# Performance work log

Measured on AMD Instinct MI355X. Metric: run time of the kernel, lower is better.

## Reference

```python
import jax, jax.numpy as jnp
import numpy as np

B, S = 2, 2048
DIM_IN, DIM_OUT, NUM_HEADS, DIM_QK = 1024, 128, 16, 128


def setup_inputs() -> dict:
    key = jax.random.key(0)
    k0, k1, k2, k3 = jax.random.split(key, 4)
    x = jax.random.normal(k0, (B, S, DIM_IN), jnp.float32)
    mask = jax.random.bernoulli(k1, 0.1, (B, S))  # True = masked-out token
    # xavier-normal-ish scales (exact init values are irrelevant for correctness)
    std_in = float(np.sqrt(2.0 / (NUM_HEADS * DIM_QK + DIM_IN * DIM_QK)))
    proj_in = jax.random.normal(k2, (DIM_IN, NUM_HEADS, 2 * DIM_QK + DIM_OUT), jnp.float32) * std_in
    v_bias = jnp.zeros((NUM_HEADS, DIM_OUT), jnp.float32)
    std_out = float(np.sqrt(2.0 / (DIM_OUT * DIM_OUT + NUM_HEADS * DIM_OUT)))
    proj_out = jax.random.normal(k3, (NUM_HEADS, DIM_OUT, DIM_OUT), jnp.float32) * std_out
    proj_out_bias = jnp.zeros((DIM_OUT,), jnp.float32)
    return {"x": x, "mask": mask, "proj_in": proj_in, "v_bias": v_bias,
            "proj_out": proj_out, "proj_out_bias": proj_out_bias}


def _rotary(t):
    # t: [z, s, h, d]; GPT-NeoX style rotary as in the torch Rotary module
    d = t.shape[-1]
    half = -(-d // 2)  # ceil(d/2), matches torch.arange(0,-1,-2/d)
    freq_half = 10000.0 ** (jnp.arange(half, dtype=jnp.float32) * (-2.0 / d))
    freq = jnp.concatenate([freq_half, freq_half[: half - d % 2]])  # length d
    pos = jnp.arange(t.shape[1], dtype=jnp.float32)
    ang = pos[:, None] * freq[None, :]             # [s, d]
    cos = jnp.cos(ang)[None, :, None, :]
    sin = jnp.sin(ang)[None, :, None, :]
    x1, x2 = jnp.split(t, 2, axis=-1)
    rot = jnp.concatenate([-x2, x1], axis=-1)
    return t * cos + rot * sin


def _inf_cube(t):
    return t ** 3


def reference(x, mask, proj_in, v_bias, proj_out, proj_out_bias):
    qkv = jnp.einsum('zki,iho->zkho', x, proj_in)
    q, k, v = jnp.split(qkv, [DIM_QK, 2 * DIM_QK], axis=-1)
    q = _rotary(q)
    k = _rotary(k)
    scores = jnp.einsum('zqha,zkha->zqkh', q, k) / jnp.sqrt(jnp.float32(DIM_QK))
    # dual mask: row (query) OR column (key) masked -> -inf
    m = jnp.logical_or(mask[:, :, None, None], mask[:, None, :, None])  # [z,q,k,1]
    scores = jnp.where(m, -jnp.inf, scores)
    attn = jnp.nan_to_num(jax.nn.softmax(scores, axis=2))  # softmax over k; nan rows -> 0
    o = jnp.einsum('zqkh,zkhx->zqhx', attn, v + v_bias[None, None])
    out = jnp.einsum('zqhx,hxy->zqy', _inf_cube(o), proj_out) + proj_out_bias[None, None]
    return _inf_cube(out)
```

## Files before the change

### kernel.cpp

```cpp
#include <hip/hip_runtime.h>
#include <math.h>

#define BZ 2
#define SQ 2048
#define DIN 1024
#define HH 16
#define NT 6144
#define MROWS 4096
#define KOUT 2048
#define KSPLIT 16

typedef unsigned short u16t;
typedef unsigned int u32t;
typedef __attribute__((ext_vector_type(8))) short bf16x8;
typedef __attribute__((ext_vector_type(4))) float f32x4;

__device__ __forceinline__ float cubef(float x) { return x * x * x; }

__device__ __forceinline__ u16t f2bf(float f) {
    u32t b = __float_as_uint(f);
    b += 0x7FFFu + ((b >> 16) & 1u);
    return (u16t)(b >> 16);
}
__device__ __forceinline__ float bf2f(u16t u) { return __uint_as_float(((u32t)u) << 16); }
__device__ __forceinline__ u32t pk2(float a, float b) {
    return (u32t)f2bf(a) | ((u32t)f2bf(b) << 16);
}

#if __has_builtin(__builtin_amdgcn_exp2f)
#define EXP2(x) __builtin_amdgcn_exp2f(x)
#else
#define EXP2(x) exp2f(x)
#endif

__device__ __forceinline__ void load_lds16(const void* g, void* l) {
    __builtin_amdgcn_global_load_lds((const __attribute__((address_space(1))) void*)g,
                                     (__attribute__((address_space(3))) void*)l, 16, 0, 0);
}

__global__ __launch_bounds__(256) void bf16_x(const float* __restrict__ x,
                                              u16t* __restrict__ xb) {
    const size_t idx = ((size_t)blockIdx.x * 256 + threadIdx.x) * 8;
    float4 f0 = *(const float4*)&x[idx];
    float4 f1 = *(const float4*)&x[idx + 4];
    u32t h[4];
    h[0] = pk2(f0.x, f0.y); h[1] = pk2(f0.z, f0.w);
    h[2] = pk2(f1.x, f1.y); h[3] = pk2(f1.z, f1.w);
    *(uint4*)&xb[idx] = *(uint4*)&h[0];
}

__global__ __launch_bounds__(256) void transpose_w(const float* __restrict__ W,
                                                   u16t* __restrict__ Th) {
    __shared__ float tile[64][68];
    const int n0 = blockIdx.x * 64;
    const int k0 = blockIdx.y * 64;
    const int t = threadIdx.x;
    {
        const int r = t >> 4, c = (t & 15) * 4;
        #pragma unroll
        for (int p = 0; p < 4; p++) {
            float4 v = *(const float4*)&W[(size_t)(k0 + r + p * 16) * NT + n0 + c];
            *(float4*)&tile[r + p * 16][c] = v;
        }
    }
    __syncthreads();
    const int nr = t >> 2;
    const int kc = (t & 3) * 16;
    u32t hi[8];
    #pragma unroll
    for (int j = 0; j < 8; j++)
        hi[j] = pk2(tile[kc + 2 * j][nr], tile[kc + 2 * j + 1][nr]);
    size_t ob = (size_t)(n0 + nr) * DIN + k0 + kc;
    *(uint4*)&Th[ob]     = *(uint4*)&hi[0];
    *(uint4*)&Th[ob + 8] = *(uint4*)&hi[4];
}

__global__ __launch_bounds__(256) void transpose_w2(const float* __restrict__ W,
                                                    u16t* __restrict__ Th) {
    __shared__ float tile[64][68];
    const int n0 = blockIdx.x * 64;
    const int k0 = blockIdx.y * 64;
    const int t = threadIdx.x;
    {
        const int r = t >> 4, c = (t & 15) * 4;
        #pragma unroll
        for (int p = 0; p < 4; p++) {
            float4 v = *(const float4*)&W[(size_t)(k0 + r + p * 16) * 128 + n0 + c];
            *(float4*)&tile[r + p * 16][c] = v;
        }
    }
    __syncthreads();
    const int nr = t >> 2;
    const int kc = (t & 3) * 16;
    u32t hi[8];
    #pragma unroll
    for (int j = 0; j < 8; j++)
        hi[j] = pk2(tile[kc + 2 * j][nr], tile[kc + 2 * j + 1][nr]);
    size_t ob = (size_t)(n0 + nr) * KOUT + k0 + kc;
    *(uint4*)&Th[ob]     = *(uint4*)&hi[0];
    *(uint4*)&Th[ob + 8] = *(uint4*)&hi[4];
}

__global__ __launch_bounds__(256) void gemm_qkv4(const u16t* __restrict__ Ah,
                                                 const u16t* __restrict__ Bh,
                                                 const float* __restrict__ vb,
                                                 u16t* __restrict__ QB,
                                                 u16t* __restrict__ KB,
                                                 u16t* __restrict__ VF) {
    __shared__ __align__(16) u16t as_h[2][4096];
    __shared__ __align__(16) u16t bs_h[2][4096];

    const int t = threadIdx.x;
    const int lane = t & 63, wid = t >> 6;
    const int quad = lane >> 4, l15 = lane & 15;
    const int wm = (wid & 1) * 64;
    const int wn = (wid >> 1) * 64;
    const int tile = blockIdx.x;
    const int h = tile / 3, t3 = tile - h * 3;
    const int colBase = tile * 128;
    const int rowBase = blockIdx.y * 128;
    const int sm = t & 127;
    const int skh = t >> 7;

    f32x4 acc[4][4];
    #pragma unroll
    for (int i = 0; i < 4; i++)
        #pragma unroll
        for (int j = 0; j < 4; j++) acc[i][j] = (f32x4){0.f, 0.f, 0.f, 0.f};

    const u16t* aPtr = Ah + (size_t)(rowBase + sm) * DIN + skh * 16;
    const u16t* bPtr = Bh + (size_t)(colBase + sm) * DIN + skh * 16;
    const int wbase = (wid >> 1) * 2048 + (wid & 1) * 512;

    load_lds16(aPtr,     &as_h[0][wbase]);
    load_lds16(aPtr + 8, &as_h[0][wbase + 1024]);
    load_lds16(bPtr,     &bs_h[0][wbase]);
    load_lds16(bPtr + 8, &bs_h[0][wbase + 1024]);

    for (int it = 0; it < 32; it++) {
        const int buf = it & 1;
        __syncthreads();
        if (it < 31) {
            const int k0 = (it + 1) * 32;
            load_lds16(aPtr + k0,     &as_h[buf ^ 1][wbase]);
            load_lds16(aPtr + k0 + 8, &as_h[buf ^ 1][wbase + 1024]);
            load_lds16(bPtr + k0,     &bs_h[buf ^ 1][wbase]);
            load_lds16(bPtr + k0 + 8, &bs_h[buf ^ 1][wbase + 1024]);
        }
        bf16x8 ah[4], bh[4];
        #pragma unroll
        for (int mt = 0; mt < 4; mt++)
            ah[mt] = *(const bf16x8*)&as_h[buf][quad * 1024 + (wm + mt * 16 + l15) * 8];
        #pragma unroll
        for (int nt = 0; nt < 4; nt++)
            bh[nt] = *(const bf16x8*)&bs_h[buf][quad * 1024 + (wn + nt * 16 + l15) * 8];
        #pragma unroll
        for (int mt = 0; mt < 4; mt++)
            #pragma unroll
            for (int nt = 0; nt < 4; nt++)
                acc[mt][nt] = __builtin_amdgcn_mfma_f32_16x16x32_bf16(ah[mt], bh[nt], acc[mt][nt], 0, 0, 0);
        __syncthreads();
    }

    const int z = rowBase >> 11;
    const int s0 = (rowBase & 2047) + wm + quad * 4;
    const size_t obase = (size_t)(z * 16 + h) * 2048;
    if (t3 == 2) {
        #pragma unroll
        for (int nt = 0; nt < 4; nt++) {
            int c = wn + nt * 16 + l15;
            float bb = vb[h * 128 + c];
            #pragma unroll
            for (int mt = 0; mt < 4; mt++)
                #pragma unroll
                for (int r = 0; r < 4; r++)
                    VF[(obase + s0 + mt * 16 + r) * 128 + c] = f2bf(acc[mt][nt][r] + bb);
        }
    } else {
        u16t* dst = t3 ? KB : QB;
        #pragma unroll
        for (int nt = 0; nt < 4; nt++) {
            int c = wn + nt * 16 + l15;
            #pragma unroll
            for (int mt = 0; mt < 4; mt++)
                #pragma unroll
                for (int r = 0; r < 4; r++)
                    dst[(obase + s0 + mt * 16 + r) * 128 + c] = f2bf(acc[mt][nt][r]);
        }
    }
}

#define QSC 0.12751744f

__global__ __launch_bounds__(256) void prep_rot_trans(u16t* __restrict__ QB,
                                                      u16t* __restrict__ KB,
                                                      u16t* __restrict__ VTh) {
    const int bx = blockIdx.x;
    const int st = bx & 63, h = (bx >> 6) & 15, z = bx >> 10;
    const int t = threadIdx.x;
    const size_t base = ((size_t)(z * 16 + h) * 2048 + st * 32) * 128;

    {
        const int r = t >> 3, w = t & 7;
        const int c = w & 3;
        const int s = st * 32 + r;
        u16t* buf = (w < 4) ? QB : KB;
        const float sc = (w < 4) ? QSC : 1.0f;
        u16t* p1 = buf + base + (size_t)r * 128 + c * 16;
        u16t* p2 = p1 + 64;
        uint4 a0 = *(uint4*)p1, a1 = *(uint4*)(p1 + 8);
        uint4 b0 = *(uint4*)p2, b1 = *(uint4*)(p2 + 8);
        u32t A[8] = {a0.x, a0.y, a0.z, a0.w, a1.x, a1.y, a1.z, a1.w};
        u32t B[8] = {b0.x, b0.y, b0.z, b0.w, b1.x, b1.y, b1.z, b1.w};
        u32t OA[8], OB[8];
        #pragma unroll
        for (int p = 0; p < 8; p++) {
            float x1a = bf2f((u16t)(A[p] & 0xFFFFu)), x1b = bf2f((u16t)(A[p] >> 16));
            float x2a = bf2f((u16t)(B[p] & 0xFFFFu)), x2b = bf2f((u16t)(B[p] >> 16));
            int j0 = c * 16 + 2 * p;
            float f0 = expf(-0.14391156831212788f * (float)j0);
            float f1 = expf(-0.14391156831212788f * (float)(j0 + 1));
            float sn0, cs0, sn1, cs1;
            sincosf((float)s * f0, &sn0, &cs0);
            sincosf((float)s * f1, &sn1, &cs1);
            sn0 *= sc; cs0 *= sc; sn1 *= sc; cs1 *= sc;
            OA[p] = pk2(x1a * cs0 - x2a * sn0, x1b * cs1 - x2b * sn1);
            OB[p] = pk2(x2a * cs0 + x1a * sn0, x2b * cs1 + x1b * sn1);
        }
        *(uint4*)p1       = make_uint4(OA[0], OA[1], OA[2], OA[3]);
        *(uint4*)(p1 + 8) = make_uint4(OA[4], OA[5], OA[6], OA[7]);
        *(uint4*)p2       = make_uint4(OB[0], OB[1], OB[2], OB[3]);
        *(uint4*)(p2 + 8) = make_uint4(OB[4], OB[5], OB[6], OB[7]);
    }

    __shared__ u16t vt[128 * 40];
    {
        uint4 a = *(uint4*)(VTh + base + t * 16);
        uint4 b = *(uint4*)(VTh + base + t * 16 + 8);
        int row = t >> 3, d0 = (t & 7) * 16;
        int prow = 2 * (row & 15) + (row >> 4);
        u32t W[8] = {a.x, a.y, a.z, a.w, b.x, b.y, b.z, b.w};
        #pragma unroll
        for (int p = 0; p < 8; p++) {
            vt[(d0 + 2 * p) * 40 + prow]     = (u16t)(W[p] & 0xFFFFu);
            vt[(d0 + 2 * p + 1) * 40 + prow] = (u16t)(W[p] >> 16);
        }
    }
    __syncthreads();
    {
        int d = t >> 1, k0 = (t & 1) * 16;
        uint4 a = *(uint4*)&vt[d * 40 + k0];
        uint4 b = *(uint4*)&vt[d * 40 + k0 + 8];
        *(uint4*)(VTh + base + t * 16)     = a;
        *(uint4*)(VTh + base + t * 16 + 8) = b;
    }
}

__global__ __launch_bounds__(256, 2) void attn_kernel8(const u16t* __restrict__ QB,
                                                       const u16t* __restrict__ KB,
                                                       const u16t* __restrict__ VTh,
                                                       const int* __restrict__ mask,
                                                       u16t* __restrict__ O3b) {
    const int blk = blockIdx.x;
    const int qt = blk & 15;
    const int h  = (blk >> 4) & 15;
    const int z  = blk >> 8;
    const int t  = threadIdx.x;
    const int lane = t & 63, wid = t >> 6;
    const int quad = lane >> 4, l15 = lane & 15;

    __shared__ __align__(16) u16t ks[2][32 * 136];
    __shared__ __align__(16) u16t vth[2][128 * 40];
    __shared__ __align__(16) u16t wlb[128 * 40];
    __shared__ int km[2][32];

    const int q0 = qt * 128;
    const size_t zh = (size_t)(z * 16 + h);
    const u16t* qb  = QB  + zh * 262144;
    const u16t* kb  = KB  + zh * 262144;
    const u16t* vhg = VTh + zh * 262144;

    bf16x8 qf[2][4];
    #pragma unroll
    for (int i = 0; i < 2; i++)
        #pragma unroll
        for (int kk = 0; kk < 4; kk++)
            qf[i][kk] = *(const bf16x8*)(qb + (size_t)(q0 + 16 * (2 * wid + i) + l15) * 128 + kk * 32 + quad * 8);

    int4 qm4[2];
    #pragma unroll
    for (int i = 0; i < 2; i++)
        qm4[i] = *(const int4*)&mask[z * SQ + q0 + 16 * (2 * wid + i) + 4 * quad];
    const int qmr[2][4] = {{qm4[0].x, qm4[0].y, qm4[0].z, qm4[0].w},
                           {qm4[1].x, qm4[1].y, qm4[1].z, qm4[1].w}};
    int rowoff[2];
    #pragma unroll
    for (int i = 0; i < 2; i++) rowoff[i] = (16 * (2 * wid + i) + 4 * quad) * 40;

    const int srow = t >> 3, sco = (t & 7) * 16;
    const int sdd = t >> 1, sk0 = (t & 1) * 16;

    uint4 ka, kb2, va, vb2;
    int kmv = 0;
    {
        ka  = *(const uint4*)(kb + t * 16);
        kb2 = *(const uint4*)(kb + t * 16 + 8);
        va  = *(const uint4*)(vhg + t * 16);
        vb2 = *(const uint4*)(vhg + t * 16 + 8);
        if (t < 32) kmv = mask[z * SQ + t];
    }

    f32x4 acc[2][8];
    #pragma unroll
    for (int i = 0; i < 2; i++)
        #pragma unroll
        for (int d = 0; d < 8; d++) acc[i][d] = (f32x4){0.f, 0.f, 0.f, 0.f};
    float dsum[2][4] = {{0.f, 0.f, 0.f, 0.f}, {0.f, 0.f, 0.f, 0.f}};

    for (int it = 0; it < 64; it++) {
        const int buf = it & 1;
        *(uint4*)&ks[buf][srow * 136 + sco]     = ka;
        *(uint4*)&ks[buf][srow * 136 + sco + 8] = kb2;
        *(uint4*)&vth[buf][sdd * 40 + sk0]      = va;
        *(uint4*)&vth[buf][sdd * 40 + sk0 + 8]  = vb2;
        if (t < 32) km[buf][t] = kmv;

        __syncthreads();

        {
            const int ktn = (it < 63) ? (it + 1) * 32 : it * 32;
            const u16t* src = kb + (size_t)ktn * 128 + t * 16;
            ka  = *(const uint4*)(src);
            kb2 = *(const uint4*)(src + 8);
            const u16t* srch = vhg + (size_t)(ktn >> 5) * 4096 + t * 16;
            va  = *(const uint4*)(srch);
            vb2 = *(const uint4*)(srch + 8);
            if (t < 32) kmv = mask[z * SQ + ktn + t];
        }

        f32x4 s4[2][2];
        #pragma unroll
        for (int i = 0; i < 2; i++)
            #pragma unroll
            for (int n = 0; n < 2; n++) s4[i][n] = (f32x4){0.f, 0.f, 0.f, 0.f};
        #pragma unroll
        for (int kk = 0; kk < 4; kk++) {
            bf16x8 kf0 = *(const bf16x8*)&ks[buf][l15 * 136 + kk * 32 + quad * 8];
            bf16x8 kf1 = *(const bf16x8*)&ks[buf][(16 + l15) * 136 + kk * 32 + quad * 8];
            s4[0][0] = __builtin_amdgcn_mfma_f32_16x16x32_bf16(qf[0][kk], kf0, s4[0][0], 0, 0, 0);
            s4[0][1] = __builtin_amdgcn_mfma_f32_16x16x32_bf16(qf[0][kk], kf1, s4[0][1], 0, 0, 0);
            s4[1][0] = __builtin_amdgcn_mfma_f32_16x16x32_bf16(qf[1][kk], kf0, s4[1][0], 0, 0, 0);
            s4[1][1] = __builtin_amdgcn_mfma_f32_16x16x32_bf16(qf[1][kk], kf1, s4[1][1], 0, 0, 0);
        }
        {
            int colm0 = km[buf][l15], colm1 = km[buf][16 + l15];
            #pragma unroll
            for (int i = 0; i < 2; i++)
                #pragma unroll
                for (int r = 0; r < 4; r++) {
                    float w0 = (qmr[i][r] | colm0) ? 0.f : EXP2(s4[i][0][r]);
                    float w1 = (qmr[i][r] | colm1) ? 0.f : EXP2(s4[i][1][r]);
                    dsum[i][r] += w0 + w1;
                    u32t pkw;
                    asm("v_cvt_pk_bf16_f32 %0, %1, %2" : "=v"(pkw) : "v"(w0), "v"(w1));
                    *(u32t*)&wlb[rowoff[i] + r * 40 + 2 * l15] = pkw;
                }
        }
        bf16x8 pa[2];
        #pragma unroll
        for (int i = 0; i < 2; i++)
            pa[i] = *(const bf16x8*)&wlb[(16 * (2 * wid + i) + l15) * 40 + quad * 8];
        #pragma unroll
        for (int dt = 0; dt < 8; dt++) {
            bf16x8 vh = *(const bf16x8*)&vth[buf][(16 * dt + l15) * 40 + quad * 8];
            acc[0][dt] = __builtin_amdgcn_mfma_f32_16x16x32_bf16(pa[0], vh, acc[0][dt], 0, 0, 0);
            acc[1][dt] = __builtin_amdgcn_mfma_f32_16x16x32_bf16(pa[1], vh, acc[1][dt], 0, 0, 0);
        }
    }

    #pragma unroll
    for (int i = 0; i < 2; i++)
        #pragma unroll
        for (int r = 0; r < 4; r++) {
            float v = dsum[i][r];
            v += __shfl_xor(v, 1);
            v += __shfl_xor(v, 2);
            v += __shfl_xor(v, 4);
            v += __shfl_xor(v, 8);
            dsum[i][r] = v;
        }

    #pragma unroll
    for (int i = 0; i < 2; i++)
        #pragma unroll
        for (int r = 0; r < 4; r++) {
            int row = 16 * (2 * wid + i) + 4 * quad + r;
            float inv = dsum[i][r] > 0.f ? 1.f / dsum[i][r] : 0.f;
            u16t* dst = O3b + (size_t)(z * SQ + q0 + row) * KOUT + h * 128;
            #pragma unroll
            for (int dt = 0; dt < 8; dt++)
                dst[16 * dt + l15] = f2bf(cubef(acc[i][dt][r] * inv));
        }
}

__global__ __launch_bounds__(256) void final_gemm3(const u16t* __restrict__ Ab,
                                                   const u16t* __restrict__ Bh,
                                                   float* __restrict__ part) {
    __shared__ __align__(16) u16t as_h[2][4 * 128 * 8];
    __shared__ __align__(16) u16t bs_h[2][4 * 128 * 8];

    const int t = threadIdx.x;
    const int lane = t & 63, wid = t >> 6;
    const int quad = lane >> 4, l15 = lane & 15;
    const int wm = (wid & 1) * 64;
    const int wn = (wid >> 1) * 64;
    const int rowBase = blockIdx.x * 128;
    const int kBase   = blockIdx.y * (KOUT / KSPLIT);
    const int sm = t & 127;
    const int skh = t >> 7;

    f32x4 acc[4][4];
    #pragma unroll
    for (int i = 0; i < 4; i++)
        #pragma unroll
        for (int j = 0; j < 4; j++) acc[i][j] = (f32x4){0.f, 0.f, 0.f, 0.f};

    const u16t* aPtr = Ab + (size_t)(rowBase + sm) * KOUT + kBase + skh * 16;
    const u16t* bPtr = Bh + (size_t)sm * KOUT + kBase + skh * 16;
    const int swoff = (skh * 2) * 1024 + sm * 8;

    uint4 a0 = *(const uint4*)(aPtr);
    uint4 a1 = *(const uint4*)(aPtr + 8);
    uint4 b0 = *(const uint4*)(bPtr);
    uint4 b1 = *(const uint4*)(bPtr + 8);

    const int NIT = (KOUT / KSPLIT) / 32;
    for (int it = 0; it < NIT; it++) {
        const int buf = it & 1;
        *(uint4*)(&as_h[buf][swoff])        = a0;
        *(uint4*)(&as_h[buf][swoff + 1024]) = a1;
        *(uint4*)(&bs_h[buf][swoff])        = b0;
        *(uint4*)(&bs_h[buf][swoff + 1024]) = b1;
        __syncthreads();
        {
            const int k0 = (it < NIT - 1) ? (it + 1) * 32 : it * 32;
            a0 = *(const uint4*)(aPtr + k0);
            a1 = *(const uint4*)(aPtr + k0 + 8);
            b0 = *(const uint4*)(bPtr + k0);
            b1 = *(const uint4*)(bPtr + k0 + 8);
        }
        bf16x8 ah[4], bh[4];
        #pragma unroll
        for (int mt = 0; mt < 4; mt++)
            ah[mt] = *(const bf16x8*)&as_h[buf][quad * 1024 + (wm + mt * 16 + l15) * 8];
        #pragma unroll
        for (int nt = 0; nt < 4; nt++)
            bh[nt] = *(const bf16x8*)&bs_h[buf][quad * 1024 + (wn + nt * 16 + l15) * 8];
        #pragma unroll
        for (int mt = 0; mt < 4; mt++)
            #pragma unroll
            for (int nt = 0; nt < 4; nt++)
                acc[mt][nt] = __builtin_amdgcn_mfma_f32_16x16x32_bf16(ah[mt], bh[nt], acc[mt][nt], 0, 0, 0);
    }

    float* pbase = part + (size_t)blockIdx.y * ((size_t)MROWS * 128);
    #pragma unroll
    for (int mt = 0; mt < 4; mt++)
        #pragma unroll
        for (int nt = 0; nt < 4; nt++) {
            int col = wn + nt * 16 + l15;
            #pragma unroll
            for (int r = 0; r < 4; r++) {
                int row = rowBase + wm + mt * 16 + quad * 4 + r;
                pbase[(size_t)row * 128 + col] = acc[mt][nt][r];
            }
        }
}

__global__ __launch_bounds__(256) void reduce_bias_cube(const float* __restrict__ part,
                                                        const float* __restrict__ bias,
                                                        float* __restrict__ out) {
    const int idx = (blockIdx.x * 256 + threadIdx.x) * 4;
    float4 s = {0.f, 0.f, 0.f, 0.f};
    #pragma unroll
    for (int p = 0; p < KSPLIT; p++) {
        float4 v = *(const float4*)&part[(size_t)p * ((size_t)MROWS * 128) + idx];
        s.x += v.x; s.y += v.y; s.z += v.z; s.w += v.w;
    }
    float4 b = *(const float4*)&bias[idx & 127];
    float4 r;
    r.x = cubef(s.x + b.x);
    r.y = cubef(s.y + b.y);
    r.z = cubef(s.z + b.z);
    r.w = cubef(s.w + b.w);
    *(float4*)&out[idx] = r;
}

extern "C" void kernel_launch(void* const* d_in, const int* in_sizes, int n_in,
                              void* d_out, int out_size, void* d_ws, size_t ws_size,
                              hipStream_t stream) {
    const float* x        = (const float*)d_in[0];
    const int*   mask     = (const int*)d_in[1];
    const float* proj_in  = (const float*)d_in[2];
    const float* v_bias   = (const float*)d_in[3];
    const float* proj_out = (const float*)d_in[4];
    const float* po_bias  = (const float*)d_in[5];
    float* out = (float*)d_out;

    u16t* QB  = (u16t*)d_ws;
    u16t* KB  = QB + (size_t)8388608;
    u16t* VTh = KB + (size_t)8388608;
    u16t* xb  = VTh + (size_t)8388608;
    u16t* O3b = xb + (size_t)4194304;
    u16t* pTh = O3b;
    u16t* WTh = QB;
    float* partials = (float*)(WTh + (size_t)128 * KOUT);

    bf16_x<<<(MROWS * DIN) / (256 * 8), 256, 0, stream>>>(x, xb);
    transpose_w<<<dim3(NT / 64, DIN / 64), 256, 0, stream>>>(proj_in, pTh);
    gemm_qkv4<<<dim3(48, MROWS / 128), 256, 0, stream>>>(xb, pTh, v_bias, QB, KB, VTh);
    prep_rot_trans<<<BZ * HH * (SQ / 32), 256, 0, stream>>>(QB, KB, VTh);
    attn_kernel8<<<BZ * HH * (SQ / 128), 256, 0, stream>>>(QB, KB, VTh, mask, O3b);
    transpose_w2<<<dim3(2, KOUT / 64), 256, 0, stream>>>(proj_out, WTh);
    final_gemm3<<<dim3(MROWS / 128, KSPLIT), 256, 0, stream>>>(O3b, WTh, partials);
    reduce_bias_cube<<<(MROWS * 128) / (256 * 4), 256, 0, stream>>>(partials, po_bias, out);
}
```

Measured before the change: 319.9 us.

## Fuse rotary and V transpose into QKV GEMM epilogue with precomputed rope table

Removes the separate prep_rot_trans kernel. The QKV GEMM now stages its output tile in LDS and applies rotary (scaled for Q) or the V transpose-permute directly before writing to global memory. Sin and cos values come from a small precomputed table instead of being recomputed per element. The GEMM grid is also remapped into grouped tiles for better L2 reuse. This saves a full read and write pass over Q, K and V, at the cost of a larger LDS footprint and an extra small kernel launch.

```diff
diff --git a/kernel.cpp b/kernel.cpp
--- a/kernel.cpp
+++ b/kernel.cpp
@@ -49,6 +49,15 @@
     *(uint4*)&xb[idx] = *(uint4*)&h[0];
 }
 
+__global__ __launch_bounds__(256) void rope_table(float* __restrict__ tab) {
+    const int idx = blockIdx.x * 256 + threadIdx.x;
+    const int s = idx >> 6, d = idx & 63;
+    float f = expf(-0.14391156831212788f * (float)d);
+    float sn, cs;
+    sincosf((float)s * f, &sn, &cs);
+    ((float2*)tab)[idx] = make_float2(cs, sn);
+}
+
 __global__ __launch_bounds__(256) void transpose_w(const float* __restrict__ W,
                                                    u16t* __restrict__ Th) {
     __shared__ float tile[64][68];
@@ -101,24 +110,31 @@
     *(uint4*)&Th[ob + 8] = *(uint4*)&hi[4];
 }
 
-__global__ __launch_bounds__(256) void gemm_qkv4(const u16t* __restrict__ Ah,
+#define QSC 0.12751744f
+
+__global__ __launch_bounds__(256) void gemm_qkv5(const u16t* __restrict__ Ah,
                                                  const u16t* __restrict__ Bh,
                                                  const float* __restrict__ vb,
+                                                 const float* __restrict__ ropetab,
                                                  u16t* __restrict__ QB,
                                                  u16t* __restrict__ KB,
-                                                 u16t* __restrict__ VF) {
-    __shared__ __align__(16) u16t as_h[2][4096];
-    __shared__ __align__(16) u16t bs_h[2][4096];
+                                                 u16t* __restrict__ VTh) {
+    __shared__ __align__(16) u16t smem[17408];
 
     const int t = threadIdx.x;
     const int lane = t & 63, wid = t >> 6;
     const int quad = lane >> 4, l15 = lane & 15;
     const int wm = (wid & 1) * 64;
     const int wn = (wid >> 1) * 64;
-    const int tile = blockIdx.x;
-    const int h = tile / 3, t3 = tile - h * 3;
-    const int colBase = tile * 128;
-    const int rowBase = blockIdx.y * 128;
+
+    const int f = blockIdx.y * 48 + blockIdx.x;
+    const int L = (f & 7) * 192 + (f >> 3);
+    const int rect = L / 48, rrem = L - rect * 48;
+    const int tileI = (rect & 7) * 6 + rrem % 6;
+    const int rowIdx = (rect >> 3) * 8 + rrem / 6;
+    const int h = tileI / 3, t3 = tileI - h * 3;
+    const int colBase = tileI * 128;
+    const int rowBase = rowIdx * 128;
     const int sm = t & 127;
     const int skh = t >> 7;
 
@@ -132,28 +148,30 @@
     const u16t* bPtr = Bh + (size_t)(colBase + sm) * DIN + skh * 16;
     const int wbase = (wid >> 1) * 2048 + (wid & 1) * 512;
 
-    load_lds16(aPtr,     &as_h[0][wbase]);
-    load_lds16(aPtr + 8, &as_h[0][wbase + 1024]);
-    load_lds16(bPtr,     &bs_h[0][wbase]);
-    load_lds16(bPtr + 8, &bs_h[0][wbase + 1024]);
+    load_lds16(aPtr,     &smem[wbase]);
+    load_lds16(aPtr + 8, &smem[wbase + 1024]);
+    load_lds16(bPtr,     &smem[8192 + wbase]);
+    load_lds16(bPtr + 8, &smem[8192 + wbase + 1024]);
+    __syncthreads();
 
     for (int it = 0; it < 32; it++) {
         const int buf = it & 1;
-        __syncthreads();
+        const int ab = buf * 4096, bb_ = 8192 + buf * 4096;
         if (it < 31) {
             const int k0 = (it + 1) * 32;
-            load_lds16(aPtr + k0,     &as_h[buf ^ 1][wbase]);
-            load_lds16(aPtr + k0 + 8, &as_h[buf ^ 1][wbase + 1024]);
-            load_lds16(bPtr + k0,     &bs_h[buf ^ 1][wbase]);
-            load_lds16(bPtr + k0 + 8, &bs_h[buf ^ 1][wbase + 1024]);
+            const int nab = (buf ^ 1) * 4096, nbb = 8192 + (buf ^ 1) * 4096;
+            load_lds16(aPtr + k0,     &smem[nab + wbase]);
+            load_lds16(aPtr + k0 + 8, &smem[nab + wbase + 1024]);
+            load_lds16(bPtr + k0,     &smem[nbb + wbase]);
+            load_lds16(bPtr + k0 + 8, &smem[nbb + wbase + 1024]);
         }
         bf16x8 ah[4], bh[4];
         #pragma unroll
         for (int mt = 0; mt < 4; mt++)
-            ah[mt] = *(const bf16x8*)&as_h[buf][quad * 1024 + (wm + mt * 16 + l15) * 8];
+            ah[mt] = *(const bf16x8*)&smem[ab + quad * 1024 + (wm + mt * 16 + l15) * 8];
         #pragma unroll
         for (int nt = 0; nt < 4; nt++)
-            bh[nt] = *(const bf16x8*)&bs_h[buf][quad * 1024 + (wn + nt * 16 + l15) * 8];
+            bh[nt] = *(const bf16x8*)&smem[bb_ + quad * 1024 + (wn + nt * 16 + l15) * 8];
         #pragma unroll
         for (int mt = 0; mt < 4; mt++)
             #pragma unroll
@@ -163,96 +181,88 @@
     }
 
     const int z = rowBase >> 11;
-    const int s0 = (rowBase & 2047) + wm + quad * 4;
-    const size_t obase = (size_t)(z * 16 + h) * 2048;
+    const int s0local = rowBase & 2047;
+    const size_t zh = (size_t)(z * 16 + h);
+    u16t* tl = smem;
+
     if (t3 == 2) {
         #pragma unroll
         for (int nt = 0; nt < 4; nt++) {
-            int c = wn + nt * 16 + l15;
-            float bb = vb[h * 128 + c];
+            float bbv = vb[h * 128 + wn + nt * 16 + l15];
             #pragma unroll
             for (int mt = 0; mt < 4; mt++)
                 #pragma unroll
                 for (int r = 0; r < 4; r++)
-                    VF[(obase + s0 + mt * 16 + r) * 128 + c] = f2bf(acc[mt][nt][r] + bb);
+                    tl[(wm + mt * 16 + quad * 4 + r) * 136 + wn + nt * 16 + l15] =
+                        f2bf(acc[mt][nt][r] + bbv);
         }
     } else {
-        u16t* dst = t3 ? KB : QB;
-        #pragma unroll
-        for (int nt = 0; nt < 4; nt++) {
-            int c = wn + nt * 16 + l15;
+        #pragma unroll
+        for (int nt = 0; nt < 4; nt++)
             #pragma unroll
             for (int mt = 0; mt < 4; mt++)
                 #pragma unroll
                 for (int r = 0; r < 4; r++)
-                    dst[(obase + s0 + mt * 16 + r) * 128 + c] = f2bf(acc[mt][nt][r]);
-        }
-    }
-}
-
-#define QSC 0.12751744f
-
-__global__ __launch_bounds__(256) void prep_rot_trans(u16t* __restrict__ QB,
-                                                      u16t* __restrict__ KB,
-                                                      u16t* __restrict__ VTh) {
-    const int bx = blockIdx.x;
-    const int st = bx & 63, h = (bx >> 6) & 15, z = bx >> 10;
-    const int t = threadIdx.x;
-    const size_t base = ((size_t)(z * 16 + h) * 2048 + st * 32) * 128;
-
-    {
-        const int r = t >> 3, w = t & 7;
-        const int c = w & 3;
-        const int s = st * 32 + r;
-        u16t* buf = (w < 4) ? QB : KB;
-        const float sc = (w < 4) ? QSC : 1.0f;
-        u16t* p1 = buf + base + (size_t)r * 128 + c * 16;
-        u16t* p2 = p1 + 64;
-        uint4 a0 = *(uint4*)p1, a1 = *(uint4*)(p1 + 8);
-        uint4 b0 = *(uint4*)p2, b1 = *(uint4*)(p2 + 8);
-        u32t A[8] = {a0.x, a0.y, a0.z, a0.w, a1.x, a1.y, a1.z, a1.w};
-        u32t B[8] = {b0.x, b0.y, b0.z, b0.w, b1.x, b1.y, b1.z, b1.w};
-        u32t OA[8], OB[8];
-        #pragma unroll
-        for (int p = 0; p < 8; p++) {
-            float x1a = bf2f((u16t)(A[p] & 0xFFFFu)), x1b = bf2f((u16t)(A[p] >> 16));
-            float x2a = bf2f((u16t)(B[p] & 0xFFFFu)), x2b = bf2f((u16t)(B[p] >> 16));
-            int j0 = c * 16 + 2 * p;
-            float f0 = expf(-0.14391156831212788f * (float)j0);
-            float f1 = expf(-0.14391156831212788f * (float)(j0 + 1));
-            float sn0, cs0, sn1, cs1;
-            sincosf((float)s * f0, &sn0, &cs0);
-            sincosf((float)s * f1, &sn1, &cs1);
-            sn0 *= sc; cs0 *= sc; sn1 *= sc; cs1 *= sc;
-            OA[p] = pk2(x1a * cs0 - x2a * sn0, x1b * cs1 - x2b * sn1);
-            OB[p] = pk2(x2a * cs0 + x1a * sn0, x2b * cs1 + x1b * sn1);
-        }
-        *(uint4*)p1       = make_uint4(OA[0], OA[1], OA[2], OA[3]);
-        *(uint4*)(p1 + 8) = make_uint4(OA[4], OA[5], OA[6], OA[7]);
-        *(uint4*)p2       = make_uint4(OB[0], OB[1], OB[2], OB[3]);
-        *(uint4*)(p2 + 8) = make_uint4(OB[4], OB[5], OB[6], OB[7]);
-    }
-
-    __shared__ u16t vt[128 * 40];
-    {
-        uint4 a = *(uint4*)(VTh + base + t * 16);
-        uint4 b = *(uint4*)(VTh + base + t * 16 + 8);
-        int row = t >> 3, d0 = (t & 7) * 16;
-        int prow = 2 * (row & 15) + (row >> 4);
-        u32t W[8] = {a.x, a.y, a.z, a.w, b.x, b.y, b.z, b.w};
-        #pragma unroll
-        for (int p = 0; p < 8; p++) {
-            vt[(d0 + 2 * p) * 40 + prow]     = (u16t)(W[p] & 0xFFFFu);
-            vt[(d0 + 2 * p + 1) * 40 + prow] = (u16t)(W[p] >> 16);
-        }
+                    tl[(wm + mt * 16 + quad * 4 + r) * 136 + wn + nt * 16 + l15] =
+                        f2bf(acc[mt][nt][r]);
     }
     __syncthreads();
-    {
-        int d = t >> 1, k0 = (t & 1) * 16;
-        uint4 a = *(uint4*)&vt[d * 40 + k0];
-        uint4 b = *(uint4*)&vt[d * 40 + k0 + 8];
-        *(uint4*)(VTh + base + t * 16)     = a;
-        *(uint4*)(VTh + base + t * 16 + 8) = b;
+
+    if (t3 != 2) {
+        u16t* dstQK = (t3 ? KB : QB) + zh * 262144;
+        const float sc = t3 ? 1.0f : QSC;
+        const int rr = t >> 2;
+        const int ch = (t & 3) << 4;
+        #pragma unroll
+        for (int half = 0; half < 2; half++) {
+            const int row = rr + half * 64;
+            const int s = s0local + row;
+            const u16t* trow = &tl[row * 136];
+            uint4 X1  = *(const uint4*)&trow[ch];
+            uint4 X1b = *(const uint4*)&trow[ch + 8];
+            uint4 X2  = *(const uint4*)&trow[ch + 64];
+            uint4 X2b = *(const uint4*)&trow[ch + 72];
+            u32t A_[8] = {X1.x, X1.y, X1.z, X1.w, X1b.x, X1b.y, X1b.z, X1b.w};
+            u32t B_[8] = {X2.x, X2.y, X2.z, X2.w, X2b.x, X2b.y, X2b.z, X2b.w};
+            u32t OA[8], OB[8];
+            const float4* tb = (const float4*)&ropetab[(size_t)s * 128 + ch * 2];
+            #pragma unroll
+            for (int p = 0; p < 8; p++) {
+                float4 tt = tb[p];
+                float cs0 = tt.x * sc, sn0 = tt.y * sc;
+                float cs1 = tt.z * sc, sn1 = tt.w * sc;
+                float x1a = bf2f((u16t)(A_[p] & 0xFFFFu)), x1b = bf2f((u16t)(A_[p] >> 16));
+                float x2a = bf2f((u16t)(B_[p] & 0xFFFFu)), x2b = bf2f((u16t)(B_[p] >> 16));
+                OA[p] = pk2(x1a * cs0 - x2a * sn0, x1b * cs1 - x2b * sn1);
+                OB[p] = pk2(x2a * cs0 + x1a * sn0, x2b * cs1 + x1b * sn1);
+            }
+            u16t* d0 = dstQK + (size_t)s * 128 + ch;
+            *(uint4*)d0        = make_uint4(OA[0], OA[1], OA[2], OA[3]);
+            *(uint4*)(d0 + 8)  = make_uint4(OA[4], OA[5], OA[6], OA[7]);
+            *(uint4*)(d0 + 64) = make_uint4(OB[0], OB[1], OB[2], OB[3]);
+            *(uint4*)(d0 + 72) = make_uint4(OB[4], OB[5], OB[6], OB[7]);
+        }
+    } else {
+        u16t* dstV = VTh + zh * 262144 + (size_t)(s0local >> 5) * 4096;
+        const int d = t & 127;
+        const int g0 = t >> 7;
+        #pragma unroll
+        for (int gg = 0; gg < 2; gg++) {
+            const int g = g0 + 2 * gg;
+            const u16t* col = &tl[(g * 32) * 136 + d];
+            u32t H[16];
+            #pragma unroll
+            for (int m = 0; m < 16; m++) {
+                u32t lo = col[m * 136];
+                u32t hi = col[(m + 16) * 136];
+                H[m] = lo | (hi << 16);
+            }
+            u16t* dv = dstV + (size_t)g * 4096 + d * 32;
+            *(uint4*)&dv[0]  = *(uint4*)&H[0];
+            *(uint4*)&dv[8]  = *(uint4*)&H[4];
+            *(uint4*)&dv[16] = *(uint4*)&H[8];
+            *(uint4*)&dv[24] = *(uint4*)&H[12];
+        }
     }
 }
 
@@ -513,13 +523,14 @@
     u16t* xb  = VTh + (size_t)8388608;
     u16t* O3b = xb + (size_t)4194304;
     u16t* pTh = O3b;
+    float* ropetab = (float*)(O3b + (size_t)6291456);
     u16t* WTh = QB;
     float* partials = (float*)(WTh + (size_t)128 * KOUT);
 
     bf16_x<<<(MROWS * DIN) / (256 * 8), 256, 0, stream>>>(x, xb);
+    rope_table<<<(SQ * 64) / 256, 256, 0, stream>>>(ropetab);
     transpose_w<<<dim3(NT / 64, DIN / 64), 256, 0, stream>>>(proj_in, pTh);
-    gemm_qkv4<<<dim3(48, MROWS / 128), 256, 0, stream>>>(xb, pTh, v_bias, QB, KB, VTh);
-    prep_rot_trans<<<BZ * HH * (SQ / 32), 256, 0, stream>>>(QB, KB, VTh);
+    gemm_qkv5<<<dim3(48, MROWS / 128), 256, 0, stream>>>(xb, pTh, v_bias, ropetab, QB, KB, VTh);
     attn_kernel8<<<BZ * HH * (SQ / 128), 256, 0, stream>>>(QB, KB, VTh, mask, O3b);
     transpose_w2<<<dim3(2, KOUT / 64), 256, 0, stream>>>(proj_out, WTh);
     final_gemm3<<<dim3(MROWS / 128, KSPLIT), 256, 0, stream>>>(O3b, WTh, partials);
```

Result: faster. 310.4 us (-2.9%).
